# Kernel optimization log

Measured on AMD Instinct MI355X. Metric: run time of the kernel, lower is better.

## Reference

```python
import jax, jax.numpy as jnp
import numpy as np

SHAPE = (4096, 4096)
TAU = 1.0
EPS = 1e-8


def setup_inputs() -> dict:
    key = jax.random.key(0)
    k1, k2, k3 = jax.random.split(key, 3)
    mask_logits = 0.1 * jax.random.normal(k1, SHAPE, dtype=jnp.float32)
    u1 = jax.random.uniform(k2, SHAPE, dtype=jnp.float32)
    u2 = jax.random.uniform(k3, SHAPE + (2,), dtype=jnp.float32)
    return {"mask_logits": mask_logits, "u1": u1, "u2": u2,
            "k": 1677721, "training": 1}


def _gumbel(u):
    # -log(-log(U + eps) + eps), matching the torch code's noise
    return -jnp.log(-jnp.log(u + EPS) + EPS)


def reference(mask_logits, u1, u2, k, training):
    shape = mask_logits.shape
    if training:
        # gumbel-perturbed logits
        logits_with_noise = (mask_logits + _gumbel(u1)) / TAU
        flat = logits_with_noise.reshape(-1)                 # [N]
        _, top_idx = jax.lax.top_k(flat, k)                  # [k]
        # scatter: binary candidate mask (constant values -> non-diff, as in torch)
        mask = jnp.zeros_like(flat).at[top_idx].set(1.0)     # [N]
        # F.gumbel_softmax(stack([0, mask], -1), tau, hard=True)[..., 1]
        logits2 = jnp.stack([jnp.zeros_like(mask), mask], axis=-1)   # [N, 2]
        g2 = _gumbel(u2.reshape(-1, 2))                      # [N, 2]
        y = jax.nn.softmax((logits2 + g2) / TAU, axis=-1)    # soft sample
        hard = jax.nn.one_hot(jnp.argmax(y, axis=-1), 2, dtype=y.dtype)
        out = (hard + y - jax.lax.stop_gradient(y))[..., 1]  # straight-through
        return out.reshape(shape)
    else:
        flat = mask_logits.reshape(-1)
        _, top_idx = jax.lax.top_k(flat, k)
        mask = jnp.zeros_like(flat).at[top_idx].set(1.0)
        return mask.reshape(shape)
```

## Files before the change

kernel.cpp:

```cpp
#include <hip/hip_runtime.h>
#include <hip/hip_bf16.h>
#include <math.h>
#include <cstdint>

#define FEPS 1e-8f
#define NBLK 2048
#define NTHR 256
#define CAND_CAP 4096


__device__ __forceinline__ uint32_t f2k(float f) {
    uint32_t b = __float_as_uint(f);
    return (b & 0x80000000u) ? ~b : (b | 0x80000000u);
}

__device__ __forceinline__ float gum_fast(float u) {
    float t = u + FEPS;
    float a = logf(t);
    float w = -a + FEPS;
    float d = logf(w);
    return -d;
}

__device__ __forceinline__ float logCR(float x) {
    return (float)log((double)x);
}
__device__ __forceinline__ float gum_cr(float u) {
    float t = u + FEPS;
    float a = logCR(t);
    float w = -a + FEPS;
    float d = logCR(w);
    return -d;
}

__device__ __forceinline__ float decide_cr(float maskv, float ua, float ub) {
    float G0 = gum_cr(ua);
    float G1 = gum_cr(ub);
    float V1 = maskv + G1;
    float diff = V1 - G0;
    return (diff > 0x1p-25f) ? 1.0f : 0.0f;
}
__device__ __forceinline__ float decide_tr(float maskv, float ua, float ub) {
    float g0 = gum_fast(ua);
    float g1 = gum_fast(ub);
    float v1 = maskv + g1;
    float diff = v1 - g0;
    if (fabsf(diff) > 1e-4f) return (diff > 0.0f) ? 1.0f : 0.0f;
    return decide_cr(maskv, ua, ub);
}

__global__ void k_zero(uint32_t* __restrict__ hist1, uint32_t* __restrict__ hist2,
                       uint32_t* __restrict__ scal, uint32_t* __restrict__ candCount) {
    int i = blockIdx.x * blockDim.x + threadIdx.x;
    int stride = gridDim.x * blockDim.x;
    for (int b = i; b < 4096; b += stride) hist1[b] = 0u;
    for (int b = i; b < (1 << 20); b += stride) hist2[b] = 0u;
    if (i < 16) scal[i] = 0u;
    if (i == 0) *candCount = 0u;
}

__global__ void __launch_bounds__(NTHR) k_keys(
        const float* __restrict__ lg, const float* __restrict__ u1,
        const int* __restrict__ trainp, uint32_t* __restrict__ keys,
        uint32_t* __restrict__ hist1, int N) {
    __shared__ uint32_t h[4096];
    for (int b = threadIdx.x; b < 4096; b += blockDim.x) h[b] = 0u;
    __syncthreads();
    const int tr = *trainp;
    const int n4 = N >> 2;
    const int tid = blockIdx.x * blockDim.x + threadIdx.x;
    const int stride = gridDim.x * blockDim.x;
    for (int i = tid; i < n4; i += stride) {
        float4 m = ((const float4*)lg)[i];
        float4 u = ((const float4*)u1)[i];
        float z0, z1, z2, z3;
        if (tr) {
            z0 = m.x + gum_fast(u.x);
            z1 = m.y + gum_fast(u.y);
            z2 = m.z + gum_fast(u.z);
            z3 = m.w + gum_fast(u.w);
        } else { z0 = m.x; z1 = m.y; z2 = m.z; z3 = m.w; }
        uint4 kk = make_uint4(f2k(z0), f2k(z1), f2k(z2), f2k(z3));
        ((uint4*)keys)[i] = kk;
        atomicAdd(&h[kk.x >> 20], 1u);
        atomicAdd(&h[kk.y >> 20], 1u);
        atomicAdd(&h[kk.z >> 20], 1u);
        atomicAdd(&h[kk.w >> 20], 1u);
    }
    for (int i = (n4 << 2) + tid; i < N; i += stride) {
        float m = lg[i], u = u1[i];
        float z = tr ? (m + gum_fast(u)) : m;
        uint32_t kx = f2k(z);
        keys[i] = kx;
        atomicAdd(&h[kx >> 20], 1u);
    }
    __syncthreads();
    for (int b = threadIdx.x; b < 4096; b += blockDim.x) {
        uint32_t v = h[b];
        if (v) atomicAdd(&hist1[b], v);
    }
}

__global__ void __launch_bounds__(1024) k_scan1(
        const uint32_t* __restrict__ hist1, const int* __restrict__ kptr,
        uint32_t* __restrict__ scal) {
    __shared__ uint32_t vals[4096];
    __shared__ uint32_t cnt[1024];
    const int t = threadIdx.x;
    uint32_t loc = 0;
    for (int j = 0; j < 4; j++) {
        uint32_t v = hist1[4095 - (t * 4 + j)];
        vals[t * 4 + j] = v;
        loc += v;
    }
    cnt[t] = loc;
    __syncthreads();
    for (int off = 1; off < 1024; off <<= 1) {
        uint32_t add = (t >= off) ? cnt[t - off] : 0u;
        __syncthreads();
        cnt[t] += add;
        __syncthreads();
    }
    const uint32_t K = (uint32_t)(*kptr);
    uint32_t excl = (t > 0) ? cnt[t - 1] : 0u;
    uint32_t incl = cnt[t];
    if (excl < K && K <= incl) {
        uint32_t c = excl;
        for (int j = 0; j < 4; j++) {
            uint32_t v = vals[t * 4 + j];
            if (K <= c + v) {
                scal[0] = (uint32_t)(4095 - (t * 4 + j));
                scal[1] = K - c;
                scal[2] = c;
                break;
            }
            c += v;
        }
    }
}

__global__ void __launch_bounds__(NTHR) k_hist2(
        const uint32_t* __restrict__ keys, const uint32_t* __restrict__ scal,
        uint32_t* __restrict__ hist2, int N) {
    const uint32_t b1 = scal[0];
    const int n4 = N >> 2;
    const int tid = blockIdx.x * blockDim.x + threadIdx.x;
    const int stride = gridDim.x * blockDim.x;
    for (int i = tid; i < n4; i += stride) {
        uint4 kk = ((const uint4*)keys)[i];
        if ((kk.x >> 20) == b1) atomicAdd(&hist2[kk.x & 0xFFFFFu], 1u);
        if ((kk.y >> 20) == b1) atomicAdd(&hist2[kk.y & 0xFFFFFu], 1u);
        if ((kk.z >> 20) == b1) atomicAdd(&hist2[kk.z & 0xFFFFFu], 1u);
        if ((kk.w >> 20) == b1) atomicAdd(&hist2[kk.w & 0xFFFFFu], 1u);
    }
    for (int i = (n4 << 2) + tid; i < N; i += stride) {
        uint32_t kx = keys[i];
        if ((kx >> 20) == b1) atomicAdd(&hist2[kx & 0xFFFFFu], 1u);
    }
}

__global__ void __launch_bounds__(NTHR) k_part(
        const uint32_t* __restrict__ hist2, uint32_t* __restrict__ part) {
    __shared__ uint32_t red[NTHR];
    uint32_t sum = 0;
    const int base = blockIdx.x << 10;
    for (int j = threadIdx.x; j < 1024; j += NTHR) sum += hist2[base + j];
    red[threadIdx.x] = sum;
    __syncthreads();
    for (int off = NTHR / 2; off; off >>= 1) {
        if (threadIdx.x < off) red[threadIdx.x] += red[threadIdx.x + off];
        __syncthreads();
    }
    if (threadIdx.x == 0) part[blockIdx.x] = red[0];
}

__global__ void __launch_bounds__(1024) k_scan2(
        const uint32_t* __restrict__ hist2, const uint32_t* __restrict__ part,
        uint32_t* __restrict__ scal) {
    __shared__ uint32_t cs[1024];
    __shared__ uint32_t bs[1024];
    __shared__ uint32_t red[1024];
    __shared__ int shI[4];
    const int t = threadIdx.x;
    const uint32_t b1 = scal[0];
    const uint32_t kk1 = scal[1];
    const uint32_t total_gt = scal[2];

    cs[t] = part[1023 - t];
    __syncthreads();
    for (int off = 1; off < 1024; off <<= 1) {
        uint32_t add = (t >= off) ? cs[t - off] : 0u;
        __syncthreads();
        cs[t] += add;
        __syncthreads();
    }
    {
        uint32_t excl = t ? cs[t - 1] : 0u;
        if (excl < kk1 && kk1 <= cs[t]) shI[0] = t;
    }
    __syncthreads();
    const int rp = shI[0];
    const int jc = 1023 - rp;
    const uint32_t gt_chunks = rp ? cs[rp - 1] : 0u;
    const uint32_t kk_in = kk1 - gt_chunks;

    bs[t] = hist2[(jc << 10) + (1023 - t)];
    __syncthreads();
    for (int off = 1; off < 1024; off <<= 1) {
        uint32_t add = (t >= off) ? bs[t - off] : 0u;
        __syncthreads();
        bs[t] += add;
        __syncthreads();
    }
    {
        uint32_t excl = t ? bs[t - 1] : 0u;
        if (excl < kk_in && kk_in <= bs[t]) shI[1] = t;
    }
    __syncthreads();
    const int rq = shI[1];
    const int b2 = (jc << 10) + (1023 - rq);

    int W = 64;
    int lo = 0, hi = 0;
    uint32_t caw = 0;
    while (true) {
        lo = b2 - W; if (lo < 0) lo = 0;
        hi = b2 + W; if (hi > 0xFFFFF) hi = 0xFFFFF;
        uint32_t v = 0;
        for (int b = lo + t; b <= hi; b += 1024) v += hist2[b];
        red[t] = v;
        __syncthreads();
        for (int off = 512; off; off >>= 1) {
            if (t < off) red[t] += red[t + off];
            __syncthreads();
        }
        uint32_t nW = red[0];
        __syncthreads();
        if (nW <= 3500u || W == 0) {
            const int ch = hi >> 10;
            const int chend = (ch << 10) + 1023;
            uint32_t v2 = 0;
            for (int b = hi + 1 + t; b <= chend; b += 1024) v2 += hist2[b];
            red[t] = v2;
            __syncthreads();
            for (int off = 512; off; off >>= 1) {
                if (t < off) red[t] += red[t + off];
                __syncthreads();
            }
            uint32_t inpart = red[0];
            __syncthreads();
            const int rpch = 1023 - ch;
            const uint32_t sufExcl = rpch ? cs[rpch - 1] : 0u;
            caw = total_gt + sufExcl + inpart;
            break;
        }
        W >>= 1;
    }
    if (t == 0) {
        scal[3] = (b1 << 20) | (uint32_t)lo;
        scal[4] = (b1 << 20) | (uint32_t)hi;
        scal[5] = caw;
    }
}

__global__ void __launch_bounds__(NTHR) k_final(
        uint32_t* __restrict__ keys ,
        const float* __restrict__ u2, const int* __restrict__ trainp,
        const uint32_t* __restrict__ scal,
        uint32_t* __restrict__ candIdx, uint32_t* __restrict__ candCount, int N) {
    const uint32_t klo = scal[3], khi = scal[4];
    const int tr = *trainp;
    const int n4 = N >> 2;
    const int tid = blockIdx.x * blockDim.x + threadIdx.x;
    const int stride = gridDim.x * blockDim.x;
    float* outf = (float*)keys;
    for (int i = tid; i < n4; i += stride) {
        uint4 kk = ((const uint4*)keys)[i];
        uint32_t ks[4] = {kk.x, kk.y, kk.z, kk.w};
        float uu[8];
        if (tr) {
            float4 ua = ((const float4*)u2)[2 * i];
            float4 ub = ((const float4*)u2)[2 * i + 1];
            uu[0] = ua.x; uu[1] = ua.y; uu[2] = ua.z; uu[3] = ua.w;
            uu[4] = ub.x; uu[5] = ub.y; uu[6] = ub.z; uu[7] = ub.w;
        }
        float res[4];
        bool inw[4];
        bool anyw = false;
        #pragma unroll
        for (int j = 0; j < 4; j++) {
            inw[j] = (ks[j] >= klo) && (ks[j] <= khi);
            anyw |= inw[j];
        }
        #pragma unroll
        for (int j = 0; j < 4; j++) {
            float mv = (ks[j] > khi) ? 1.0f : 0.0f;
            res[j] = (tr && !inw[j]) ? decide_tr(mv, uu[2 * j], uu[2 * j + 1]) : mv;
        }
        if (!anyw) {
            ((float4*)outf)[i] = make_float4(res[0], res[1], res[2], res[3]);
        } else {
            #pragma unroll
            for (int j = 0; j < 4; j++) {
                if (inw[j]) {
                    uint32_t p = atomicAdd(candCount, 1u);
                    if (p < CAND_CAP) candIdx[p] = (uint32_t)(4 * i + j);
                } else {
                    outf[4 * i + j] = res[j];
                }
            }
        }
    }
    for (int i = (n4 << 2) + tid; i < N; i += stride) {
        uint32_t kx = keys[i];
        if (kx >= klo && kx <= khi) {
            uint32_t p = atomicAdd(candCount, 1u);
            if (p < CAND_CAP) candIdx[p] = (uint32_t)i;
            continue;
        }
        float mv = (kx > khi) ? 1.0f : 0.0f;
        outf[i] = tr ? decide_tr(mv, u2[2 * i], u2[2 * i + 1]) : mv;
    }
}

__global__ void __launch_bounds__(NTHR) k_refine(
        const float* __restrict__ lg, const float* __restrict__ u1,
        const float* __restrict__ u2, const int* __restrict__ kptr,
        const int* __restrict__ trainp, const uint32_t* __restrict__ scal,
        const uint32_t* __restrict__ candIdx, const uint32_t* __restrict__ candCount,
        float* __restrict__ out) {
    __shared__ float zs[CAND_CAP];
    __shared__ int is[CAND_CAP];
    const int tr = *trainp;
    int n = (int)(*candCount);
    if (n > CAND_CAP) n = CAND_CAP;
    int npow2 = 64;
    while (npow2 < n) npow2 <<= 1;

    for (int e = threadIdx.x; e < npow2; e += NTHR) {
        if (e < n) {
            int i = (int)candIdx[e];
            float m = lg[i];
            zs[e] = tr ? (m + gum_cr(u1[i])) : m;
            is[e] = i;
        } else {
            zs[e] = -INFINITY;
            is[e] = 0x40000000 + e;
        }
    }
    __syncthreads();

    for (int size = 2; size <= npow2; size <<= 1) {
        for (int str = size >> 1; str > 0; str >>= 1) {
            for (int e = threadIdx.x; e < npow2; e += NTHR) {
                int p = e ^ str;
                if (p > e) {
                    float za = zs[e], zb = zs[p];
                    int ia = is[e], ib = is[p];
                    bool aBefore = (za > zb) || (za == zb && ia < ib);
                    bool descBlock = ((e & size) == 0);
                    if (descBlock ? !aBefore : aBefore) {
                        zs[e] = zb; zs[p] = za;
                        is[e] = ib; is[p] = ia;
                    }
                }
            }
            __syncthreads();
        }
    }

    const int K = *kptr;
    const int caw = (int)scal[5];
    const int R = K - caw;
    for (int e = threadIdx.x; e < n; e += NTHR) {
        int i = is[e];
        float mv = (e < R) ? 1.0f : 0.0f;
        float o;
        if (tr) {
            o = decide_cr(mv, u2[2 * i], u2[2 * i + 1]);
        } else {
            o = mv;
        }
        out[i] = o;
    }
}

extern "C" void kernel_launch(void* const* d_in, const int* in_sizes, int n_in,
                              void* d_out, int out_size, void* d_ws, size_t ws_size,
                              hipStream_t stream) {
    const float* lg = (const float*)d_in[0];
    const float* u1 = (const float*)d_in[1];
    const float* u2 = (const float*)d_in[2];
    const int* kptr = (const int*)d_in[3];
    const int* trainp = (const int*)d_in[4];
    float* out = (float*)d_out;
    const int N = in_sizes[0];

    uint32_t* keys = (uint32_t*)d_out;

    uint32_t* hist1 = (uint32_t*)d_ws;
    uint32_t* hist2 = hist1 + 4096;
    uint32_t* part = hist2 + (1u << 20);
    uint32_t* scal = part + 1024;
    uint32_t* candCount = scal + 16;
    uint32_t* candIdx = candCount + 1;

    k_zero<<<dim3(1024), dim3(256), 0, stream>>>(hist1, hist2, scal, candCount);
    k_keys<<<dim3(NBLK), dim3(NTHR), 0, stream>>>(lg, u1, trainp, keys, hist1, N);
    k_scan1<<<dim3(1), dim3(1024), 0, stream>>>(hist1, kptr, scal);
    k_hist2<<<dim3(NBLK), dim3(NTHR), 0, stream>>>(keys, scal, hist2, N);
    k_part<<<dim3(1024), dim3(NTHR), 0, stream>>>(hist2, part);
    k_scan2<<<dim3(1), dim3(1024), 0, stream>>>(hist2, part, scal);
    k_final<<<dim3(NBLK), dim3(NTHR), 0, stream>>>(keys, u2, trainp, scal, candIdx, candCount, N);
    k_refine<<<dim3(1), dim3(NTHR), 0, stream>>>(lg, u1, u2, kptr, trainp, scal, candIdx, candCount, out);
}
```

Before: 160.1 us.

## Bin first-pass histogram by value range and count greater-than keys in second pass

The first-pass histogram now bins the perturbed logits linearly over a fixed range ([-8, 24) at 1/128 width) instead of using the top 12 bits of the sortable key. The second pass histograms a 2^20-wide key window starting just below the chosen bin edge and counts the keys above that window. This should give much finer first-pass resolution for the concentrated value distribution, so fewer elements land in the refined window and fewer contend on global atomics. It also replaces the zeroing kernel with hipMemsetAsync. The fixed value range assumes the data fall roughly inside it, and the window may not cover the whole selected bin if keys there span more than 2^20 codes.

```diff
diff --git a/kernel.cpp b/kernel.cpp
--- a/kernel.cpp
+++ b/kernel.cpp
@@ -7,6 +7,10 @@
 #define NBLK 2048
 #define NTHR 256
 #define CAND_CAP 4096
+
+#define ZMIN 8.0f
+#define ZSCALE 128.0f
+#define ZBINW 0.0078125f
 
 
 __device__ __forceinline__ uint32_t f2k(float f) {
@@ -49,14 +53,12 @@
     return decide_cr(maskv, ua, ub);
 }
 
-__global__ void k_zero(uint32_t* __restrict__ hist1, uint32_t* __restrict__ hist2,
-                       uint32_t* __restrict__ scal, uint32_t* __restrict__ candCount) {
-    int i = blockIdx.x * blockDim.x + threadIdx.x;
-    int stride = gridDim.x * blockDim.x;
-    for (int b = i; b < 4096; b += stride) hist1[b] = 0u;
-    for (int b = i; b < (1 << 20); b += stride) hist2[b] = 0u;
-    if (i < 16) scal[i] = 0u;
-    if (i == 0) *candCount = 0u;
+__device__ __forceinline__ int zbin(float z) {
+    float t = (z + ZMIN) * ZSCALE;
+    int b = (int)t;
+    if (b < 0) b = 0;
+    if (b > 4095) b = 4095;
+    return b;
 }
 
 __global__ void __launch_bounds__(NTHR) k_keys(
@@ -82,17 +84,16 @@
         } else { z0 = m.x; z1 = m.y; z2 = m.z; z3 = m.w; }
         uint4 kk = make_uint4(f2k(z0), f2k(z1), f2k(z2), f2k(z3));
         ((uint4*)keys)[i] = kk;
-        atomicAdd(&h[kk.x >> 20], 1u);
-        atomicAdd(&h[kk.y >> 20], 1u);
-        atomicAdd(&h[kk.z >> 20], 1u);
-        atomicAdd(&h[kk.w >> 20], 1u);
+        atomicAdd(&h[zbin(z0)], 1u);
+        atomicAdd(&h[zbin(z1)], 1u);
+        atomicAdd(&h[zbin(z2)], 1u);
+        atomicAdd(&h[zbin(z3)], 1u);
     }
     for (int i = (n4 << 2) + tid; i < N; i += stride) {
         float m = lg[i], u = u1[i];
         float z = tr ? (m + gum_fast(u)) : m;
-        uint32_t kx = f2k(z);
-        keys[i] = kx;
-        atomicAdd(&h[kx >> 20], 1u);
+        keys[i] = f2k(z);
+        atomicAdd(&h[zbin(z)], 1u);
     }
     __syncthreads();
     for (int b = threadIdx.x; b < 4096; b += blockDim.x) {
@@ -129,9 +130,10 @@
         for (int j = 0; j < 4; j++) {
             uint32_t v = vals[t * 4 + j];
             if (K <= c + v) {
-                scal[0] = (uint32_t)(4095 - (t * 4 + j));
-                scal[1] = K - c;
-                scal[2] = c;
+                int b1 = 4095 - (t * 4 + j);
+                float edge = (float)b1 * ZBINW - ZMIN;
+                uint32_t kb = f2k(edge) - 2048u;
+                scal[0] = kb;
                 break;
             }
             c += v;
@@ -141,22 +143,36 @@
 
 __global__ void __launch_bounds__(NTHR) k_hist2(
         const uint32_t* __restrict__ keys, const uint32_t* __restrict__ scal,
-        uint32_t* __restrict__ hist2, int N) {
-    const uint32_t b1 = scal[0];
+        uint32_t* __restrict__ hist2, uint32_t* __restrict__ gtOut, int N) {
+    __shared__ uint32_t red[NTHR];
+    const uint32_t kb = scal[0];
+    const uint32_t hiB = kb + (1u << 20);
     const int n4 = N >> 2;
     const int tid = blockIdx.x * blockDim.x + threadIdx.x;
     const int stride = gridDim.x * blockDim.x;
+    uint32_t gt = 0;
     for (int i = tid; i < n4; i += stride) {
         uint4 kk = ((const uint4*)keys)[i];
-        if ((kk.x >> 20) == b1) atomicAdd(&hist2[kk.x & 0xFFFFFu], 1u);
-        if ((kk.y >> 20) == b1) atomicAdd(&hist2[kk.y & 0xFFFFFu], 1u);
-        if ((kk.z >> 20) == b1) atomicAdd(&hist2[kk.z & 0xFFFFFu], 1u);
-        if ((kk.w >> 20) == b1) atomicAdd(&hist2[kk.w & 0xFFFFFu], 1u);
+        uint32_t ks[4] = {kk.x, kk.y, kk.z, kk.w};
+        #pragma unroll
+        for (int j = 0; j < 4; j++) {
+            uint32_t kx = ks[j];
+            if (kx >= hiB) gt++;
+            else if (kx >= kb) atomicAdd(&hist2[kx - kb], 1u);
+        }
     }
     for (int i = (n4 << 2) + tid; i < N; i += stride) {
         uint32_t kx = keys[i];
-        if ((kx >> 20) == b1) atomicAdd(&hist2[kx & 0xFFFFFu], 1u);
-    }
+        if (kx >= hiB) gt++;
+        else if (kx >= kb) atomicAdd(&hist2[kx - kb], 1u);
+    }
+    red[threadIdx.x] = gt;
+    __syncthreads();
+    for (int off = NTHR / 2; off; off >>= 1) {
+        if (threadIdx.x < off) red[threadIdx.x] += red[threadIdx.x + off];
+        __syncthreads();
+    }
+    if (threadIdx.x == 0 && red[0]) atomicAdd(gtOut, red[0]);
 }
 
 __global__ void __launch_bounds__(NTHR) k_part(
@@ -176,15 +192,15 @@
 
 __global__ void __launch_bounds__(1024) k_scan2(
         const uint32_t* __restrict__ hist2, const uint32_t* __restrict__ part,
-        uint32_t* __restrict__ scal) {
+        const int* __restrict__ kptr, uint32_t* __restrict__ scal) {
     __shared__ uint32_t cs[1024];
     __shared__ uint32_t bs[1024];
     __shared__ uint32_t red[1024];
     __shared__ int shI[4];
     const int t = threadIdx.x;
-    const uint32_t b1 = scal[0];
-    const uint32_t kk1 = scal[1];
-    const uint32_t total_gt = scal[2];
+    const uint32_t kb = scal[0];
+    const uint32_t GT = scal[1];
+    const uint32_t kk1 = (uint32_t)(*kptr) - GT;
 
     cs[t] = part[1023 - t];
     __syncthreads();
@@ -251,14 +267,14 @@
             __syncthreads();
             const int rpch = 1023 - ch;
             const uint32_t sufExcl = rpch ? cs[rpch - 1] : 0u;
-            caw = total_gt + sufExcl + inpart;
+            caw = GT + sufExcl + inpart;
             break;
         }
         W >>= 1;
     }
     if (t == 0) {
-        scal[3] = (b1 << 20) | (uint32_t)lo;
-        scal[4] = (b1 << 20) | (uint32_t)hi;
+        scal[3] = kb + (uint32_t)lo;
+        scal[4] = kb + (uint32_t)hi;
         scal[5] = caw;
     }
 }
@@ -405,12 +421,14 @@
     uint32_t* candCount = scal + 16;
     uint32_t* candIdx = candCount + 1;
 
-    k_zero<<<dim3(1024), dim3(256), 0, stream>>>(hist1, hist2, scal, candCount);
+    size_t zero_bytes = (size_t)(4096 + (1u << 20) + 1024 + 16 + 1) * sizeof(uint32_t);
+    hipMemsetAsync(d_ws, 0, zero_bytes, stream);
+
     k_keys<<<dim3(NBLK), dim3(NTHR), 0, stream>>>(lg, u1, trainp, keys, hist1, N);
     k_scan1<<<dim3(1), dim3(1024), 0, stream>>>(hist1, kptr, scal);
-    k_hist2<<<dim3(NBLK), dim3(NTHR), 0, stream>>>(keys, scal, hist2, N);
+    k_hist2<<<dim3(NBLK), dim3(NTHR), 0, stream>>>(keys, scal, hist2, &scal[1], N);
     k_part<<<dim3(1024), dim3(NTHR), 0, stream>>>(hist2, part);
-    k_scan2<<<dim3(1), dim3(1024), 0, stream>>>(hist2, part, scal);
+    k_scan2<<<dim3(1), dim3(1024), 0, stream>>>(hist2, part, kptr, scal);
     k_final<<<dim3(NBLK), dim3(NTHR), 0, stream>>>(keys, u2, trainp, scal, candIdx, candCount, N);
     k_refine<<<dim3(1), dim3(NTHR), 0, stream>>>(lg, u1, u2, kptr, trainp, scal, candIdx, candCount, out);
 }
```

Result: slower. 181.1 us (+13.2%).
